# Kernel optimization log

Measured on AMD Instinct MI355X. Metric: run time of the kernel, lower is better.

Reference implementation:

```python
import jax, jax.numpy as jnp
import numpy as np

B, T, C, H = 2, 2048, 1024, 16

def setup_inputs() -> dict:
    key = jax.random.key(0)
    k1, k2, k3 = jax.random.split(key, 3)
    scale = 0.02
    return {
        "x": jax.random.normal(k1, (B, T, C), dtype=jnp.float32),
        "w_attn": jax.random.normal(k2, (C, 3 * C), dtype=jnp.float32) * scale,
        "b_attn": jnp.zeros((3 * C,), dtype=jnp.float32),
        "w_proj": jax.random.normal(k3, (C, C), dtype=jnp.float32) * scale,
        "b_proj": jnp.zeros((C,), dtype=jnp.float32),
    }

def reference(x, w_attn, b_attn, w_proj, b_proj):
    Bx, Tx, Cx = x.shape
    hd = Cx // H  # head dim
    qkv = x @ w_attn + b_attn  # [B,T,3C]
    q, k, v = jnp.split(qkv, 3, axis=-1)
    # [B,H,T,hd]
    q = q.reshape(Bx, Tx, H, hd).transpose(0, 2, 1, 3)
    k = k.reshape(Bx, Tx, H, hd).transpose(0, 2, 1, 3)
    v = v.reshape(Bx, Tx, H, hd).transpose(0, 2, 1, 3)
    att = jnp.einsum('bhqd,bhkd->bhqk', q, k) * (1.0 / jnp.sqrt(jnp.float32(hd)))
    causal = jnp.tril(jnp.ones((Tx, Tx), dtype=bool))  # [T,T]
    att = jnp.where(causal[None, None], att, jnp.float32(-jnp.inf))
    att = jax.nn.softmax(att, axis=-1)
    y = jnp.einsum('bhqk,bhkd->bhqd', att, v)  # [B,H,T,hd]
    y = y.transpose(0, 2, 1, 3).reshape(Bx, Tx, Cx)
    return y @ w_proj + b_proj
```

## Files before the change

### kernel.cpp

```cpp
#include <hip/hip_runtime.h>
#include <hip/hip_bf16.h>
#include <stdint.h>

#define B_SZ 2
#define T_SZ 2048
#define C_SZ 1024
#define H_SZ 16
#define HD   64
#define BH   (B_SZ * H_SZ)
#define M_SZ (B_SZ * T_SZ)
#define N_QKV (3 * C_SZ)

typedef __attribute__((ext_vector_type(8))) __bf16 bf16x8;
typedef __attribute__((ext_vector_type(4))) float f32x4;
typedef __attribute__((ext_vector_type(8))) unsigned short us8;
typedef __attribute__((ext_vector_type(4))) unsigned short us4;
typedef __attribute__((ext_vector_type(4))) unsigned int u32x4;

__device__ __forceinline__ unsigned short f2bf(float f) {
    unsigned int u = __builtin_bit_cast(unsigned int, f);
    u += 0x7fffu + ((u >> 16) & 1u);
    return (unsigned short)(u >> 16);
}

__device__ __forceinline__ void gll16(const unsigned short* g, unsigned short* l) {
    __builtin_amdgcn_global_load_lds(
        (const __attribute__((address_space(1))) unsigned int*)g,
        (__attribute__((address_space(3))) unsigned int*)l, 16, 0, 0);
}

__device__ __forceinline__ void hard_sync() {
    asm volatile("s_waitcnt vmcnt(0) lgkmcnt(0)" ::: "memory");
    __builtin_amdgcn_sched_barrier(0);
    __syncthreads();
}

__global__ __launch_bounds__(256) void k_prep(const float* __restrict__ x,
                                              const float* __restrict__ wa,
                                              const float* __restrict__ wp,
                                              unsigned short* __restrict__ xb,
                                              unsigned short* __restrict__ wta,
                                              unsigned short* __restrict__ wtp) {
    __shared__ float tile[32][33];
    const int tid = threadIdx.x;
    int idx = blockIdx.x;
    if (idx < 2048) {
        const size_t i = ((size_t)idx * 256 + tid) * 8;
        f32x4 a = *(const f32x4*)(x + i);
        f32x4 b = *(const f32x4*)(x + i + 4);
        us8 o;
        #pragma unroll
        for (int j = 0; j < 4; ++j) { o[j] = f2bf(a[j]); o[4 + j] = f2bf(b[j]); }
        *(us8*)(xb + i) = o;
        return;
    }
    const float* in; unsigned short* out; int N;
    if (idx < 5120) { idx -= 2048; in = wa; out = wta; N = N_QKV; }
    else            { idx -= 5120; in = wp; out = wtp; N = C_SZ; }
    const int nx = N / 32;
    const int n0 = (idx % nx) * 32, k0 = (idx / nx) * 32;
    const int tx = tid & 31, ty = tid >> 5;
    #pragma unroll
    for (int j = 0; j < 32; j += 8)
        tile[ty + j][tx] = in[(size_t)(k0 + ty + j) * N + (n0 + tx)];
    __syncthreads();
    #pragma unroll
    for (int j = 0; j < 32; j += 8)
        out[(size_t)(n0 + ty + j) * C_SZ + (k0 + tx)] = f2bf(tile[tx][ty + j]);
}

template <int EPI>
__global__ __launch_bounds__(256) void k_gemm(const unsigned short* __restrict__ A,
                                              const unsigned short* __restrict__ Bt,
                                              const float* __restrict__ bias,
                                              float* __restrict__ Cout,
                                              unsigned short* __restrict__ q_ws,
                                              unsigned short* __restrict__ k_ws,
                                              unsigned short* __restrict__ vT_ws,
                                              int M, int N, int K, int NX) {
    __shared__ __attribute__((aligned(16))) unsigned short Ald[128 * 64];
    __shared__ __attribute__((aligned(16))) unsigned short Bld[128 * 64];
    const int tid = threadIdx.x;
    const int wid = tid >> 6, lane = tid & 63;
    const int wr = wid >> 1, wc = wid & 1;
    const int g = lane >> 4, l15 = lane & 15;
    const int nwg = gridDim.x;
    const int wg = (blockIdx.x & 7) * (nwg >> 3) + (blockIdx.x >> 3);
    const int m0 = (wg / NX) * 128, n0 = (wg % NX) * 128;

    f32x4 acc[4][4];
    #pragma unroll
    for (int i = 0; i < 4; ++i)
        #pragma unroll
        for (int j = 0; j < 4; ++j) acc[i][j] = (f32x4){0.f, 0.f, 0.f, 0.f};

    for (int k0 = 0; k0 < K; k0 += 64) {
        hard_sync();
        #pragma unroll
        for (int i = 0; i < 4; ++i) {
            int c = i * 256 + tid;
            int row = c >> 3;
            int colb = ((c & 7) << 4) ^ ((row & 7) << 4);
            gll16(A  + (size_t)(m0 + row) * K + k0 + (colb >> 1), Ald + i * 2048 + wid * 512);
            gll16(Bt + (size_t)(n0 + row) * K + k0 + (colb >> 1), Bld + i * 2048 + wid * 512);
        }
        hard_sync();

        #pragma unroll
        for (int ks = 0; ks < 2; ++ks) {
            bf16x8 af[4], bfr[4];
            #pragma unroll
            for (int mi = 0; mi < 4; ++mi) {
                int row = wr * 64 + mi * 16 + l15;
                af[mi] = *(const bf16x8*)((const char*)Ald + row * 128 +
                                          ((ks * 64 + g * 16) ^ ((row & 7) << 4)));
            }
            #pragma unroll
            for (int nj = 0; nj < 4; ++nj) {
                int row = wc * 64 + nj * 16 + l15;
                bfr[nj] = *(const bf16x8*)((const char*)Bld + row * 128 +
                                           ((ks * 64 + g * 16) ^ ((row & 7) << 4)));
            }
            #pragma unroll
            for (int mi = 0; mi < 4; ++mi)
                #pragma unroll
                for (int nj = 0; nj < 4; ++nj)
                    acc[mi][nj] = __builtin_amdgcn_mfma_f32_16x16x32_bf16(
                        af[mi], bfr[nj], acc[mi][nj], 0, 0, 0);
        }
    }

    if (EPI == 0) {
        #pragma unroll
        for (int nj = 0; nj < 4; ++nj) {
            int col = n0 + wc * 64 + nj * 16 + l15;
            float bv = bias[col];
            #pragma unroll
            for (int mi = 0; mi < 4; ++mi) {
                int rowb = m0 + wr * 64 + mi * 16 + g * 4;
                #pragma unroll
                for (int r = 0; r < 4; ++r)
                    Cout[(size_t)(rowb + r) * N + col] = acc[mi][nj][r] + bv;
            }
        }
    } else {
        #pragma unroll
        for (int nj = 0; nj < 4; ++nj) {
            int col = n0 + wc * 64 + nj * 16 + l15;
            float bv = bias[col];
            int which = col >> 10;
            int c10 = col & 1023;
            int h = c10 >> 6, d = c10 & 63;
            #pragma unroll
            for (int mi = 0; mi < 4; ++mi) {
                #pragma unroll
                for (int r = 0; r < 4; ++r) {
                    int row = m0 + wr * 64 + mi * 16 + g * 4 + r;
                    int bb = row >> 11, t = row & 2047;
                    unsigned short val = f2bf(acc[mi][nj][r] + bv);
                    if (which == 2)
                        vT_ws[((size_t)(bb * H_SZ + h) * HD + d) * T_SZ + t] = val;
                    else
                        (which ? k_ws : q_ws)[((size_t)(bb * H_SZ + h) * T_SZ + t) * HD + d] = val;
                }
            }
        }
    }
}

__global__ __launch_bounds__(512) void k_attn(const unsigned short* __restrict__ q_ws,
                                              const unsigned short* __restrict__ k_ws,
                                              const unsigned short* __restrict__ vT_ws,
                                              unsigned short* __restrict__ y_ws) {
    __shared__ __attribute__((aligned(16))) unsigned short Kbuf[2][8192];
    __shared__ __attribute__((aligned(16))) unsigned short Vbuf[3][8192];
    const int tid = threadIdx.x;
    const int wid = tid >> 6, lane = tid & 63;
    const int g = lane >> 4, l15 = lane & 15;
    const int n = blockIdx.x;
    const int xcd = n & 7, j = (n >> 3) & 7, rk = n >> 6;
    const int bh = xcd + 8 * rk;
    const size_t kv_off = (size_t)bh * T_SZ * HD;
    const unsigned short* Kg = k_ws + kv_off;
    const unsigned short* Vg = vT_ws + (size_t)bh * HD * T_SZ;
    const int b = bh >> 4, h = bh & 15;
    const float SC = 0.125f * 1.44269504f;
    const int qloc = wid * 16 + l15;

    auto stageK = [&](int kv, int buf) {
        #pragma unroll
        for (int i = 0; i < 2; ++i) {
            int c = i * 512 + tid;
            int row = c >> 3;
            int colb = ((c & 7) << 4) ^ ((row & 7) << 4);
            gll16(Kg + (size_t)(kv * 128 + row) * HD + (colb >> 1),
                  &Kbuf[buf][i * 4096 + wid * 512]);
        }
    };
    auto stageV = [&](int kv, int buf) {
        #pragma unroll
        for (int i = 0; i < 2; ++i) {
            int c = i * 512 + tid;
            int row = c >> 4;
            int colb = ((c & 15) << 4) ^ ((row & 15) << 4);
            gll16(Vg + (size_t)row * T_SZ + kv * 128 + (colb >> 1),
                  &Vbuf[buf][i * 4096 + wid * 512]);
        }
    };

    #pragma unroll 1
    for (int phase = 0; phase < 2; ++phase) {
        const int qt = phase ? j : (15 - j);
        const int nkv = qt + 1;

        const int qrow = qt * 128 + wid * 16 + l15;
        bf16x8 aq[2];
        aq[0] = *(const bf16x8*)(q_ws + kv_off + (size_t)qrow * HD + g * 8);
        aq[1] = *(const bf16x8*)(q_ws + kv_off + (size_t)qrow * HD + 32 + g * 8);

        float m_run = -3e38f, l_part = 0.f;
        f32x4 acc[4];
        #pragma unroll
        for (int dt = 0; dt < 4; ++dt) acc[dt] = (f32x4){0.f, 0.f, 0.f, 0.f};
        u32x4 pfA[4], pfB[4];

        auto qk = [&](const char* Kb, f32x4 (&st)[8]) {
            __builtin_amdgcn_s_setprio(1);
            #pragma unroll
            for (int kt = 0; kt < 8; ++kt) {
                f32x4 sv = (f32x4){0.f, 0.f, 0.f, 0.f};
                #pragma unroll
                for (int ks = 0; ks < 2; ++ks) {
                    int row = kt * 16 + l15;
                    bf16x8 ak = *(const bf16x8*)(Kb + row * 128 +
                                                 ((ks * 64 + g * 16) ^ ((row & 7) << 4)));
                    sv = __builtin_amdgcn_mfma_f32_16x16x32_bf16(ak, aq[ks], sv, 0, 0, 0);
                }
                st[kt] = sv;
            }
            __builtin_amdgcn_s_setprio(0);
        };
        auto pv = [&](const char* Vb, const u32x4 (&pf)[4]) {
            __builtin_amdgcn_s_setprio(1);
            #pragma unroll
            for (int ks = 0; ks < 4; ++ks) {
                bf16x8 ap = __builtin_bit_cast(bf16x8, pf[ks]);
                #pragma unroll
                for (int dt = 0; dt < 4; ++dt) {
                    int row = dt * 16 + l15;
                    bf16x8 bv = *(const bf16x8*)(Vb + row * 256 +
                                                 ((ks * 64 + g * 16) ^ ((row & 15) << 4)));
                    acc[dt] = __builtin_amdgcn_mfma_f32_16x16x32_bf16(ap, bv, acc[dt], 0, 0, 0);
                }
            }
            __builtin_amdgcn_s_setprio(0);
        };
        auto softmax = [&](f32x4 (&st)[8], bool diag, u32x4 (&pf)[4]) {
            float t[32];
            #pragma unroll
            for (int kt = 0; kt < 8; ++kt)
                #pragma unroll
                for (int r = 0; r < 4; ++r) t[kt * 4 + r] = st[kt][r];
            if (diag) {
                #pragma unroll
                for (int kt = 0; kt < 8; ++kt)
                    #pragma unroll
                    for (int r = 0; r < 4; ++r)
                        if (kt * 16 + g * 4 + r > qloc) t[kt * 4 + r] = -3e38f;
            }
            float m16v[16];
            #pragma unroll
            for (int i2 = 0; i2 < 16; ++i2) m16v[i2] = fmaxf(t[i2], t[i2 + 16]);
            float m8v[8];
            #pragma unroll
            for (int i2 = 0; i2 < 8; ++i2) m8v[i2] = fmaxf(m16v[i2], m16v[i2 + 8]);
            float m4v[4];
            #pragma unroll
            for (int i2 = 0; i2 < 4; ++i2) m4v[i2] = fmaxf(m8v[i2], m8v[i2 + 4]);
            float mx = fmaxf(fmaxf(m4v[0], m4v[1]), fmaxf(m4v[2], m4v[3]));
            mx = fmaxf(mx, __shfl_xor(mx, 16, 64));
            mx = fmaxf(mx, __shfl_xor(mx, 32, 64));
            float mt = mx * SC;
            if (!__all(mt - m_run <= 8.0f)) {
                float mnew = fmaxf(m_run, mt);
                float alpha = exp2f(m_run - mnew);
                m_run = mnew;
                l_part *= alpha;
                float ao[4];
                #pragma unroll
                for (int r = 0; r < 4; ++r) {
                    int ai = __builtin_amdgcn_ds_bpermute((g * 4 + r) * 4,
                                                          __builtin_bit_cast(int, alpha));
                    ao[r] = __builtin_bit_cast(float, ai);
                }
                #pragma unroll
                for (int dt = 0; dt < 4; ++dt)
                    #pragma unroll
                    for (int r = 0; r < 4; ++r) acc[dt][r] *= ao[r];
            }
            float p[32];
            #pragma unroll
            for (int i2 = 0; i2 < 32; ++i2) p[i2] = exp2f(fmaf(t[i2], SC, -m_run));
            float s16v[16];
            #pragma unroll
            for (int i2 = 0; i2 < 16; ++i2) s16v[i2] = p[i2] + p[i2 + 16];
            float s8v[8];
            #pragma unroll
            for (int i2 = 0; i2 < 8; ++i2) s8v[i2] = s16v[i2] + s16v[i2 + 8];
            float s4v[4];
            #pragma unroll
            for (int i2 = 0; i2 < 4; ++i2) s4v[i2] = s8v[i2] + s8v[i2 + 4];
            l_part += (s4v[0] + s4v[1]) + (s4v[2] + s4v[3]);
            #pragma unroll
            for (int ks = 0; ks < 4; ++ks) {
                unsigned int x0, y0, x1, y1;
                asm("v_cvt_pk_bf16_f32 %0, %1, %2" : "=v"(x0) : "v"(p[8 * ks + 0]), "v"(p[8 * ks + 1]));
                asm("v_cvt_pk_bf16_f32 %0, %1, %2" : "=v"(x1) : "v"(p[8 * ks + 2]), "v"(p[8 * ks + 3]));
                asm("v_cvt_pk_bf16_f32 %0, %1, %2" : "=v"(y0) : "v"(p[8 * ks + 4]), "v"(p[8 * ks + 5]));
                asm("v_cvt_pk_bf16_f32 %0, %1, %2" : "=v"(y1) : "v"(p[8 * ks + 6]), "v"(p[8 * ks + 7]));
                asm("v_permlane32_swap_b32 %0, %1" : "+v"(x0), "+v"(y0));
                asm("v_permlane16_swap_b32 %0, %1" : "+v"(x0), "+v"(y0));
                asm("v_permlane32_swap_b32 %0, %1" : "+v"(x1), "+v"(y1));
                asm("v_permlane16_swap_b32 %0, %1" : "+v"(x1), "+v"(y1));
                pf[ks] = (u32x4){x0, x1, y0, y1};
            }
        };

        hard_sync();
        stageK(0, 0); stageV(0, 0);

        hard_sync();
        if (1 < nkv) { stageK(1, 1); stageV(1, 1); }
        {
            f32x4 st[8];
            qk((const char*)Kbuf[0], st);
            softmax(st, nkv == 1, pfA);
        }
        bool lastA = true;
        for (int i = 1; i < nkv; ) {
            hard_sync();
            if (i + 1 < nkv) { stageK(i + 1, (i + 1) & 1); stageV(i + 1, (i + 1) % 3); }
            {
                f32x4 st[8];
                qk((const char*)Kbuf[i & 1], st);
                pv((const char*)Vbuf[(i - 1) % 3], pfA);
                softmax(st, i == nkv - 1, pfB);
            }
            ++i; lastA = false; if (i == nkv) break;
            hard_sync();
            if (i + 1 < nkv) { stageK(i + 1, (i + 1) & 1); stageV(i + 1, (i + 1) % 3); }
            {
                f32x4 st[8];
                qk((const char*)Kbuf[i & 1], st);
                pv((const char*)Vbuf[(i - 1) % 3], pfB);
                softmax(st, i == nkv - 1, pfA);
            }
            ++i; lastA = true; if (i == nkv) break;
        }
        if (lastA) pv((const char*)Vbuf[(nkv - 1) % 3], pfA);
        else       pv((const char*)Vbuf[(nkv - 1) % 3], pfB);

        float lsum = l_part;
        lsum += __shfl_xor(lsum, 16, 64);
        lsum += __shfl_xor(lsum, 32, 64);
        float lo[4];
        #pragma unroll
        for (int r = 0; r < 4; ++r) {
            int li = __builtin_amdgcn_ds_bpermute((g * 4 + r) * 4,
                                                  __builtin_bit_cast(int, lsum));
            lo[r] = __builtin_bit_cast(float, li);
        }
        #pragma unroll
        for (int r = 0; r < 4; ++r) {
            int tq = qt * 128 + wid * 16 + g * 4 + r;
            float inv = 1.0f / lo[r];
            #pragma unroll
            for (int dt = 0; dt < 4; ++dt)
                y_ws[(size_t)(b * T_SZ + tq) * C_SZ + h * 64 + dt * 16 + l15] =
                    f2bf(acc[dt][r] * inv);
        }
    }
}

extern "C" void kernel_launch(void* const* d_in, const int* in_sizes, int n_in,
                              void* d_out, int out_size, void* d_ws, size_t ws_size,
                              hipStream_t stream) {
    const float* x      = (const float*)d_in[0];
    const float* w_attn = (const float*)d_in[1];
    const float* b_attn = (const float*)d_in[2];
    const float* w_proj = (const float*)d_in[3];
    const float* b_proj = (const float*)d_in[4];
    float* out = (float*)d_out;

    char* ws = (char*)d_ws;
    unsigned short* q_ws  = (unsigned short*)(ws + 0);
    unsigned short* k_ws  = (unsigned short*)(ws + 8388608);
    unsigned short* vT_ws = (unsigned short*)(ws + 16777216);
    unsigned short* wtp   = (unsigned short*)(ws + 25165824);
    unsigned short* xb    = (unsigned short*)(ws + 27262976);
    unsigned short* y_ws  = (unsigned short*)(ws + 27262976);
    unsigned short* wta   = (unsigned short*)(ws + 35651584);

    k_prep<<<dim3(6144), 256, 0, stream>>>(x, w_attn, w_proj, xb, wta, wtp);

    k_gemm<1><<<dim3((N_QKV / 128) * (M_SZ / 128)), 256, 0, stream>>>(
        xb, wta, b_attn, nullptr, q_ws, k_ws, vT_ws, M_SZ, N_QKV, C_SZ, N_QKV / 128);

    k_attn<<<dim3(256), 512, 0, stream>>>(q_ws, k_ws, vT_ws, y_ws);

    k_gemm<0><<<dim3((C_SZ / 128) * (M_SZ / 128)), 256, 0, stream>>>(
        y_ws, wtp, b_proj, out, nullptr, nullptr, nullptr, M_SZ, C_SZ, C_SZ, C_SZ / 128);
}
```

Baseline: 114.0 us.

## Halve attention query tiles to 64 rows, doubling blocks, and vectorize V-transpose stores

The attention kernel now uses 256-thread blocks that each handle 64 query rows instead of 128, launching 512 blocks with adjusted causal masking offsets and paired long/short tiles for balance. V staging switches from triple to double buffering, issuing V loads one step later and adding a barrier before the final PV. The QKV GEMM epilogue packs four consecutive bf16 values into a single 8-byte store for the transposed V layout, and GEMM dimensions become compile-time template parameters. Smaller tiles aim for better occupancy and load balance, but they re-read K/V more often and expose V load latency more.

```diff
diff --git a/kernel.cpp b/kernel.cpp
--- a/kernel.cpp
+++ b/kernel.cpp
@@ -69,15 +69,15 @@
         out[(size_t)(n0 + ty + j) * C_SZ + (k0 + tx)] = f2bf(tile[tx][ty + j]);
 }
 
-template <int EPI>
+template <int EPI, int NN, int KK>
 __global__ __launch_bounds__(256) void k_gemm(const unsigned short* __restrict__ A,
                                               const unsigned short* __restrict__ Bt,
                                               const float* __restrict__ bias,
                                               float* __restrict__ Cout,
                                               unsigned short* __restrict__ q_ws,
                                               unsigned short* __restrict__ k_ws,
-                                              unsigned short* __restrict__ vT_ws,
-                                              int M, int N, int K, int NX) {
+                                              unsigned short* __restrict__ vT_ws) {
+    constexpr int NX = NN / 128;
     __shared__ __attribute__((aligned(16))) unsigned short Ald[128 * 64];
     __shared__ __attribute__((aligned(16))) unsigned short Bld[128 * 64];
     const int tid = threadIdx.x;
@@ -94,15 +94,15 @@
         #pragma unroll
         for (int j = 0; j < 4; ++j) acc[i][j] = (f32x4){0.f, 0.f, 0.f, 0.f};
 
-    for (int k0 = 0; k0 < K; k0 += 64) {
+    for (int k0 = 0; k0 < KK; k0 += 64) {
         hard_sync();
         #pragma unroll
         for (int i = 0; i < 4; ++i) {
             int c = i * 256 + tid;
             int row = c >> 3;
             int colb = ((c & 7) << 4) ^ ((row & 7) << 4);
-            gll16(A  + (size_t)(m0 + row) * K + k0 + (colb >> 1), Ald + i * 2048 + wid * 512);
-            gll16(Bt + (size_t)(n0 + row) * K + k0 + (colb >> 1), Bld + i * 2048 + wid * 512);
+            gll16(A  + (size_t)(m0 + row) * KK + k0 + (colb >> 1), Ald + i * 2048 + wid * 512);
+            gll16(Bt + (size_t)(n0 + row) * KK + k0 + (colb >> 1), Bld + i * 2048 + wid * 512);
         }
         hard_sync();
 
@@ -140,7 +140,7 @@
                 int rowb = m0 + wr * 64 + mi * 16 + g * 4;
                 #pragma unroll
                 for (int r = 0; r < 4; ++r)
-                    Cout[(size_t)(rowb + r) * N + col] = acc[mi][nj][r] + bv;
+                    Cout[(size_t)(rowb + r) * NN + col] = acc[mi][nj][r] + bv;
             }
         }
     } else {
@@ -153,32 +153,35 @@
             int h = c10 >> 6, d = c10 & 63;
             #pragma unroll
             for (int mi = 0; mi < 4; ++mi) {
-                #pragma unroll
-                for (int r = 0; r < 4; ++r) {
-                    int row = m0 + wr * 64 + mi * 16 + g * 4 + r;
-                    int bb = row >> 11, t = row & 2047;
-                    unsigned short val = f2bf(acc[mi][nj][r] + bv);
-                    if (which == 2)
-                        vT_ws[((size_t)(bb * H_SZ + h) * HD + d) * T_SZ + t] = val;
-                    else
-                        (which ? k_ws : q_ws)[((size_t)(bb * H_SZ + h) * T_SZ + t) * HD + d] = val;
+                int row0 = m0 + wr * 64 + mi * 16 + g * 4;
+                int bb = row0 >> 11, t0 = row0 & 2047;
+                if (which == 2) {
+                    us4 pk;
+                    #pragma unroll
+                    for (int r = 0; r < 4; ++r) pk[r] = f2bf(acc[mi][nj][r] + bv);
+                    *(us4*)&vT_ws[((size_t)(bb * H_SZ + h) * HD + d) * T_SZ + t0] = pk;
+                } else {
+                    #pragma unroll
+                    for (int r = 0; r < 4; ++r)
+                        (which ? k_ws : q_ws)[((size_t)(bb * H_SZ + h) * T_SZ + t0 + r) * HD + d] =
+                            f2bf(acc[mi][nj][r] + bv);
                 }
             }
         }
     }
 }
 
-__global__ __launch_bounds__(512) void k_attn(const unsigned short* __restrict__ q_ws,
+__global__ __launch_bounds__(256) void k_attn(const unsigned short* __restrict__ q_ws,
                                               const unsigned short* __restrict__ k_ws,
                                               const unsigned short* __restrict__ vT_ws,
                                               unsigned short* __restrict__ y_ws) {
     __shared__ __attribute__((aligned(16))) unsigned short Kbuf[2][8192];
-    __shared__ __attribute__((aligned(16))) unsigned short Vbuf[3][8192];
+    __shared__ __attribute__((aligned(16))) unsigned short Vbuf[2][8192];
     const int tid = threadIdx.x;
     const int wid = tid >> 6, lane = tid & 63;
     const int g = lane >> 4, l15 = lane & 15;
     const int n = blockIdx.x;
-    const int xcd = n & 7, j = (n >> 3) & 7, rk = n >> 6;
+    const int xcd = n & 7, j = (n >> 3) & 15, rk = n >> 7;
     const int bh = xcd + 8 * rk;
     const size_t kv_off = (size_t)bh * T_SZ * HD;
     const unsigned short* Kg = k_ws + kv_off;
@@ -189,31 +192,32 @@
 
     auto stageK = [&](int kv, int buf) {
         #pragma unroll
-        for (int i = 0; i < 2; ++i) {
-            int c = i * 512 + tid;
+        for (int i = 0; i < 4; ++i) {
+            int c = i * 256 + tid;
             int row = c >> 3;
             int colb = ((c & 7) << 4) ^ ((row & 7) << 4);
             gll16(Kg + (size_t)(kv * 128 + row) * HD + (colb >> 1),
-                  &Kbuf[buf][i * 4096 + wid * 512]);
+                  &Kbuf[buf][i * 2048 + wid * 512]);
         }
     };
     auto stageV = [&](int kv, int buf) {
         #pragma unroll
-        for (int i = 0; i < 2; ++i) {
-            int c = i * 512 + tid;
+        for (int i = 0; i < 4; ++i) {
+            int c = i * 256 + tid;
             int row = c >> 4;
             int colb = ((c & 15) << 4) ^ ((row & 15) << 4);
             gll16(Vg + (size_t)row * T_SZ + kv * 128 + (colb >> 1),
-                  &Vbuf[buf][i * 4096 + wid * 512]);
+                  &Vbuf[buf][i * 2048 + wid * 512]);
         }
     };
 
     #pragma unroll 1
     for (int phase = 0; phase < 2; ++phase) {
-        const int qt = phase ? j : (15 - j);
-        const int nkv = qt + 1;
-
-        const int qrow = qt * 128 + wid * 16 + l15;
+        const int qb = phase ? j : (31 - j);
+        const int nkv = (qb + 2) >> 1;
+        const int moff = (nkv - 1) * 128 - qb * 64;
+
+        const int qrow = qb * 64 + wid * 16 + l15;
         bf16x8 aq[2];
         aq[0] = *(const bf16x8*)(q_ws + kv_off + (size_t)qrow * HD + g * 8);
         aq[1] = *(const bf16x8*)(q_ws + kv_off + (size_t)qrow * HD + 32 + g * 8);
@@ -266,7 +270,7 @@
                 for (int kt = 0; kt < 8; ++kt)
                     #pragma unroll
                     for (int r = 0; r < 4; ++r)
-                        if (kt * 16 + g * 4 + r > qloc) t[kt * 4 + r] = -3e38f;
+                        if (kt * 16 + g * 4 + r + moff > qloc) t[kt * 4 + r] = -3e38f;
             }
             float m16v[16];
             #pragma unroll
@@ -327,10 +331,11 @@
         };
 
         hard_sync();
-        stageK(0, 0); stageV(0, 0);
+        stageK(0, 0);
 
         hard_sync();
-        if (1 < nkv) { stageK(1, 1); stageV(1, 1); }
+        if (1 < nkv) stageK(1, 1);
+        stageV(0, 0);
         {
             f32x4 st[8];
             qk((const char*)Kbuf[0], st);
@@ -339,26 +344,29 @@
         bool lastA = true;
         for (int i = 1; i < nkv; ) {
             hard_sync();
-            if (i + 1 < nkv) { stageK(i + 1, (i + 1) & 1); stageV(i + 1, (i + 1) % 3); }
+            if (i + 1 < nkv) stageK(i + 1, (i + 1) & 1);
+            stageV(i, i & 1);
             {
                 f32x4 st[8];
                 qk((const char*)Kbuf[i & 1], st);
-                pv((const char*)Vbuf[(i - 1) % 3], pfA);
+                pv((const char*)Vbuf[(i - 1) & 1], pfA);
                 softmax(st, i == nkv - 1, pfB);
             }
             ++i; lastA = false; if (i == nkv) break;
             hard_sync();
-            if (i + 1 < nkv) { stageK(i + 1, (i + 1) & 1); stageV(i + 1, (i + 1) % 3); }
+            if (i + 1 < nkv) stageK(i + 1, (i + 1) & 1);
+            stageV(i, i & 1);
             {
                 f32x4 st[8];
                 qk((const char*)Kbuf[i & 1], st);
-                pv((const char*)Vbuf[(i - 1) % 3], pfB);
+                pv((const char*)Vbuf[(i - 1) & 1], pfB);
                 softmax(st, i == nkv - 1, pfA);
             }
-            ++i; lastA = true; if (i == nkv) break;
-        }
-        if (lastA) pv((const char*)Vbuf[(nkv - 1) % 3], pfA);
-        else       pv((const char*)Vbuf[(nkv - 1) % 3], pfB);
+            ++i; lastA = true;
+        }
+        hard_sync();
+        if (lastA) pv((const char*)Vbuf[(nkv - 1) & 1], pfA);
+        else       pv((const char*)Vbuf[(nkv - 1) & 1], pfB);
 
         float lsum = l_part;
         lsum += __shfl_xor(lsum, 16, 64);
@@ -372,7 +380,7 @@
         }
         #pragma unroll
         for (int r = 0; r < 4; ++r) {
-            int tq = qt * 128 + wid * 16 + g * 4 + r;
+            int tq = qb * 64 + wid * 16 + g * 4 + r;
             float inv = 1.0f / lo[r];
             #pragma unroll
             for (int dt = 0; dt < 4; ++dt)
@@ -403,11 +411,11 @@
 
     k_prep<<<dim3(6144), 256, 0, stream>>>(x, w_attn, w_proj, xb, wta, wtp);
 
-    k_gemm<1><<<dim3((N_QKV / 128) * (M_SZ / 128)), 256, 0, stream>>>(
-        xb, wta, b_attn, nullptr, q_ws, k_ws, vT_ws, M_SZ, N_QKV, C_SZ, N_QKV / 128);
-
-    k_attn<<<dim3(256), 512, 0, stream>>>(q_ws, k_ws, vT_ws, y_ws);
-
-    k_gemm<0><<<dim3((C_SZ / 128) * (M_SZ / 128)), 256, 0, stream>>>(
-        y_ws, wtp, b_proj, out, nullptr, nullptr, nullptr, M_SZ, C_SZ, C_SZ, C_SZ / 128);
-}
+    k_gemm<1, N_QKV, C_SZ><<<dim3((N_QKV / 128) * (M_SZ / 128)), 256, 0, stream>>>(
+        xb, wta, b_attn, nullptr, q_ws, k_ws, vT_ws);
+
+    k_attn<<<dim3(512), 256, 0, stream>>>(q_ws, k_ws, vT_ws, y_ws);
+
+    k_gemm<0, C_SZ, C_SZ><<<dim3((C_SZ / 128) * (M_SZ / 128)), 256, 0, stream>>>(
+        y_ws, wtp, b_proj, out, nullptr, nullptr, nullptr);
+}
```

Measured after the change: 122.5 us. +7.4%, slower.

## Double-buffer GEMM LDS tiles with K=32 stages and compile-time dims

Applied to the files above, without the earlier changes.

Restructures the GEMM main loop to use two LDS buffers of 128x32 tiles, issuing the global-to-LDS loads for the next K slice before computing the current one, so memory latency overlaps with MFMA work and one barrier per iteration is removed. It also makes N and K template constants and raises wave priority around the MFMA block. The trade-off is half the K depth per barrier, which means twice as many loop iterations and syncs, plus a narrower 4-way swizzle that may cause more LDS bank conflicts.

```diff
diff --git a/kernel.cpp b/kernel.cpp
--- a/kernel.cpp
+++ b/kernel.cpp
@@ -69,17 +69,17 @@
         out[(size_t)(n0 + ty + j) * C_SZ + (k0 + tx)] = f2bf(tile[tx][ty + j]);
 }
 
-template <int EPI>
+template <int EPI, int NN, int KK>
 __global__ __launch_bounds__(256) void k_gemm(const unsigned short* __restrict__ A,
                                               const unsigned short* __restrict__ Bt,
                                               const float* __restrict__ bias,
                                               float* __restrict__ Cout,
                                               unsigned short* __restrict__ q_ws,
                                               unsigned short* __restrict__ k_ws,
-                                              unsigned short* __restrict__ vT_ws,
-                                              int M, int N, int K, int NX) {
-    __shared__ __attribute__((aligned(16))) unsigned short Ald[128 * 64];
-    __shared__ __attribute__((aligned(16))) unsigned short Bld[128 * 64];
+                                              unsigned short* __restrict__ vT_ws) {
+    constexpr int NX = NN / 128;
+    __shared__ __attribute__((aligned(16))) unsigned short Abuf[2][128 * 32];
+    __shared__ __attribute__((aligned(16))) unsigned short Bbuf[2][128 * 32];
     const int tid = threadIdx.x;
     const int wid = tid >> 6, lane = tid & 63;
     const int wr = wid >> 1, wc = wid & 1;
@@ -94,40 +94,47 @@
         #pragma unroll
         for (int j = 0; j < 4; ++j) acc[i][j] = (f32x4){0.f, 0.f, 0.f, 0.f};
 
-    for (int k0 = 0; k0 < K; k0 += 64) {
+    auto stage = [&](int bi, int k0) {
+        #pragma unroll
+        for (int i = 0; i < 2; ++i) {
+            int c = i * 256 + tid;
+            int row = c >> 2;
+            int colb = ((c & 3) << 4) ^ ((row & 3) << 4);
+            gll16(A  + (size_t)(m0 + row) * KK + k0 + (colb >> 1),
+                  &Abuf[bi][i * 2048 + wid * 512]);
+            gll16(Bt + (size_t)(n0 + row) * KK + k0 + (colb >> 1),
+                  &Bbuf[bi][i * 2048 + wid * 512]);
+        }
+    };
+
+    stage(0, 0);
+    hard_sync();
+    int cur = 0;
+    for (int k0 = 0; k0 < KK; k0 += 32) {
+        if (k0 + 32 < KK) stage(cur ^ 1, k0 + 32);
+        bf16x8 af[4], bfr[4];
+        #pragma unroll
+        for (int mi = 0; mi < 4; ++mi) {
+            int row = wr * 64 + mi * 16 + l15;
+            af[mi] = *(const bf16x8*)((const char*)Abuf[cur] + row * 64 +
+                                      ((g * 16) ^ ((row & 3) << 4)));
+        }
+        #pragma unroll
+        for (int nj = 0; nj < 4; ++nj) {
+            int row = wc * 64 + nj * 16 + l15;
+            bfr[nj] = *(const bf16x8*)((const char*)Bbuf[cur] + row * 64 +
+                                       ((g * 16) ^ ((row & 3) << 4)));
+        }
+        __builtin_amdgcn_s_setprio(1);
+        #pragma unroll
+        for (int mi = 0; mi < 4; ++mi)
+            #pragma unroll
+            for (int nj = 0; nj < 4; ++nj)
+                acc[mi][nj] = __builtin_amdgcn_mfma_f32_16x16x32_bf16(
+                    af[mi], bfr[nj], acc[mi][nj], 0, 0, 0);
+        __builtin_amdgcn_s_setprio(0);
         hard_sync();
-        #pragma unroll
-        for (int i = 0; i < 4; ++i) {
-            int c = i * 256 + tid;
-            int row = c >> 3;
-            int colb = ((c & 7) << 4) ^ ((row & 7) << 4);
-            gll16(A  + (size_t)(m0 + row) * K + k0 + (colb >> 1), Ald + i * 2048 + wid * 512);
-            gll16(Bt + (size_t)(n0 + row) * K + k0 + (colb >> 1), Bld + i * 2048 + wid * 512);
-        }
-        hard_sync();
-
-        #pragma unroll
-        for (int ks = 0; ks < 2; ++ks) {
-            bf16x8 af[4], bfr[4];
-            #pragma unroll
-            for (int mi = 0; mi < 4; ++mi) {
-                int row = wr * 64 + mi * 16 + l15;
-                af[mi] = *(const bf16x8*)((const char*)Ald + row * 128 +
-                                          ((ks * 64 + g * 16) ^ ((row & 7) << 4)));
-            }
-            #pragma unroll
-            for (int nj = 0; nj < 4; ++nj) {
-                int row = wc * 64 + nj * 16 + l15;
-                bfr[nj] = *(const bf16x8*)((const char*)Bld + row * 128 +
-                                           ((ks * 64 + g * 16) ^ ((row & 7) << 4)));
-            }
-            #pragma unroll
-            for (int mi = 0; mi < 4; ++mi)
-                #pragma unroll
-                for (int nj = 0; nj < 4; ++nj)
-                    acc[mi][nj] = __builtin_amdgcn_mfma_f32_16x16x32_bf16(
-                        af[mi], bfr[nj], acc[mi][nj], 0, 0, 0);
-        }
+        cur ^= 1;
     }
 
     if (EPI == 0) {
@@ -140,7 +147,7 @@
                 int rowb = m0 + wr * 64 + mi * 16 + g * 4;
                 #pragma unroll
                 for (int r = 0; r < 4; ++r)
-                    Cout[(size_t)(rowb + r) * N + col] = acc[mi][nj][r] + bv;
+                    Cout[(size_t)(rowb + r) * NN + col] = acc[mi][nj][r] + bv;
             }
         }
     } else {
@@ -403,11 +410,11 @@
 
     k_prep<<<dim3(6144), 256, 0, stream>>>(x, w_attn, w_proj, xb, wta, wtp);
 
-    k_gemm<1><<<dim3((N_QKV / 128) * (M_SZ / 128)), 256, 0, stream>>>(
-        xb, wta, b_attn, nullptr, q_ws, k_ws, vT_ws, M_SZ, N_QKV, C_SZ, N_QKV / 128);
+    k_gemm<1, N_QKV, C_SZ><<<dim3((N_QKV / 128) * (M_SZ / 128)), 256, 0, stream>>>(
+        xb, wta, b_attn, nullptr, q_ws, k_ws, vT_ws);
 
     k_attn<<<dim3(256), 512, 0, stream>>>(q_ws, k_ws, vT_ws, y_ws);
 
-    k_gemm<0><<<dim3((C_SZ / 128) * (M_SZ / 128)), 256, 0, stream>>>(
-        y_ws, wtp, b_proj, out, nullptr, nullptr, nullptr, M_SZ, C_SZ, C_SZ, C_SZ / 128);
-}
+    k_gemm<0, C_SZ, C_SZ><<<dim3((C_SZ / 128) * (M_SZ / 128)), 256, 0, stream>>>(
+        y_ws, wtp, b_proj, out, nullptr, nullptr, nullptr);
+}
```

Measured after the change: 140.0 us. 1.23x slower.
